# Kernel optimization log

Hardware: AMD Instinct MI355X
Metric: run time of the kernel (lower is better)

The kernel has to match this reference:

```python
import math
import jax, jax.numpy as jnp
import numpy as np

E = 256
HEADS = 8
WS = 8
BN_EPS = 1e-5


def pos_encoding_2d(embed_dim, H, W):
    d_half = embed_dim // 2
    div = jnp.exp(jnp.arange(0, d_half, 2, dtype=jnp.float32) * (-math.log(10000.0) / d_half))
    ang_h = jnp.arange(H, dtype=jnp.float32)[:, None] * div[None, :]  # [H, d_half//2]
    pe_h = jnp.zeros((H, d_half), jnp.float32).at[:, 0::2].set(jnp.sin(ang_h)).at[:, 1::2].set(jnp.cos(ang_h))
    ang_w = jnp.arange(W, dtype=jnp.float32)[:, None] * div[None, :]
    pe_w = jnp.zeros((W, d_half), jnp.float32).at[:, 0::2].set(jnp.sin(ang_w)).at[:, 1::2].set(jnp.cos(ang_w))
    pe = jnp.concatenate([
        jnp.broadcast_to(pe_h[:, None, :], (H, W, d_half)),
        jnp.broadcast_to(pe_w[None, :, :], (H, W, d_half)),
    ], axis=-1)  # [H, W, E]
    return jnp.transpose(pe, (2, 0, 1))[None]  # [1, E, H, W]


def window_partition(x, ws):
    # x: [B, E, H, W] -> [B*Hn*Wn, ws*ws, E]
    B, e, H, W = x.shape
    Hn, Wn = H // ws, W // ws
    x = x.reshape(B, e, Hn, ws, Wn, ws)
    x = jnp.transpose(x, (0, 2, 4, 3, 5, 1))  # [B, Hn, Wn, ws, ws, E]
    return x.reshape(B * Hn * Wn, ws * ws, e)


def window_reverse(x, B, H, W, ws):
    Hn, Wn = H // ws, W // ws
    e = x.shape[-1]
    x = x.reshape(B, Hn, Wn, ws, ws, e)
    x = jnp.transpose(x, (0, 5, 1, 3, 2, 4))  # [B, E, Hn, ws, Wn, ws]
    return x.reshape(B, e, H, W)


def setup_inputs() -> dict:
    key = jax.random.key(0)
    ks = jax.random.split(key, 16)
    B, H, W = 8, 128, 128
    in_ch = (512, 256, 256)
    s = lambda fan: 1.0 / np.sqrt(fan)
    return {
        "x5": jax.random.normal(ks[0], (B, in_ch[0], H, W), jnp.float32),
        "d1": jax.random.normal(ks[1], (B, in_ch[1], H, W), jnp.float32),
        "d2": jax.random.normal(ks[2], (B, in_ch[2], H, W), jnp.float32),
        "kp_w": jax.random.normal(ks[3], (E, in_ch[0]), jnp.float32) * s(in_ch[0]),
        "qp_w": jax.random.normal(ks[4], (E, in_ch[1]), jnp.float32) * s(in_ch[1]),
        "vp_w": jax.random.normal(ks[5], (E, in_ch[2]), jnp.float32) * s(in_ch[2]),
        "sp_w": jax.random.normal(ks[6], (E, in_ch[1]), jnp.float32) * s(in_ch[1]),
        "in_proj_w": jax.random.normal(ks[7], (3 * E, E), jnp.float32) * s(E),
        "in_proj_b": jnp.zeros((3 * E,), jnp.float32),
        "out_proj_w": jax.random.normal(ks[8], (E, E), jnp.float32) * s(E),
        "out_proj_b": jnp.zeros((E,), jnp.float32),
        "post_w": jax.random.normal(ks[9], (E, 2 * E, 3, 3), jnp.float32) * s(2 * E * 9),
        "gamma": jnp.ones((E,), jnp.float32),
        "beta": jnp.zeros((E,), jnp.float32),
    }


def reference(x5, d1, d2, kp_w, qp_w, vp_w, sp_w, in_proj_w, in_proj_b,
              out_proj_w, out_proj_b, post_w, gamma, beta):
    B, _, H, W = d1.shape
    pe = pos_encoding_2d(E, H, W)

    # 1x1 projections + positional encoding
    q = jnp.einsum('bchw,ec->behw', d1, qp_w) + pe
    k = jnp.einsum('bchw,ec->behw', x5, kp_w) + pe
    v = jnp.einsum('bchw,ec->behw', d2, vp_w) + pe

    # window partition -> [N, L, E]
    qw = window_partition(q, WS)
    kw = window_partition(k, WS)
    vw = window_partition(v, WS)
    N, L, _ = qw.shape
    hd = E // HEADS

    Wq, Wk, Wv = in_proj_w[:E], in_proj_w[E:2 * E], in_proj_w[2 * E:]
    bq, bk, bv = in_proj_b[:E], in_proj_b[E:2 * E], in_proj_b[2 * E:]
    qh = (qw @ Wq.T + bq).reshape(N, L, HEADS, hd)
    kh = (kw @ Wk.T + bk).reshape(N, L, HEADS, hd)
    vh = (vw @ Wv.T + bv).reshape(N, L, HEADS, hd)

    scale = 1.0 / math.sqrt(hd)
    scores = jnp.einsum('nqhd,nkhd->nhqk', qh, kh) * scale  # [N, heads, L, L]
    attn = jax.nn.softmax(scores, axis=-1)
    o = jnp.einsum('nhqk,nkhd->nqhd', attn, vh).reshape(N, L, E)
    o = o @ out_proj_w.T + out_proj_b

    attn_out = window_reverse(o, B, H, W, WS)  # [B, E, H, W]
    skip = jnp.einsum('bchw,ec->behw', d1, sp_w)

    y = jnp.concatenate([attn_out, skip], axis=1)  # [B, 2E, H, W]
    y = jax.lax.conv_general_dilated(
        y, post_w, window_strides=(1, 1), padding=((1, 1), (1, 1)),
        dimension_numbers=('NCHW', 'OIHW', 'NCHW'))
    # BatchNorm2d, training-mode batch statistics
    mean = jnp.mean(y, axis=(0, 2, 3), keepdims=True)
    var = jnp.var(y, axis=(0, 2, 3), keepdims=True)
    y = (y - mean) * jax.lax.rsqrt(var + BN_EPS)
    y = y * gamma[None, :, None, None] + beta[None, :, None, None]
    return jax.nn.relu(y)
```

## Files before the change

kernel.cpp:

```cpp
#include <hip/hip_runtime.h>
#include <cstdio>
#include <cmath>

typedef __attribute__((ext_vector_type(8))) short bf16x8;
typedef __attribute__((ext_vector_type(4))) float f32x4;

#define MFMA16(a, b, c) __builtin_amdgcn_mfma_f32_16x16x32_bf16((a), (b), (c), 0, 0, 0)

#define WSO_PE    0u
#define WSO_WQC   65536u
#define WSO_WKC   (WSO_WQC + 131072u)
#define WSO_WVC   (WSO_WKC + 262144u)
#define WSO_WSP   (WSO_WVC + 131072u)
#define WSO_WOP   (WSO_WSP + 131072u)
#define WSO_WC    (WSO_WOP + 131072u)
#define WSO_TB    (WSO_WC + 2359296u)
#define WSO_QH    (WSO_TB + 786432u)
#define WSO_KH    (WSO_QH + 67108864u)
#define WSO_VT    (WSO_KH + 67108864u)
#define WSO_YT    (WSO_VT + 67108864u)
#define WSO_SUMS  (WSO_YT + 134217728u)
#define WSO_SC    (WSO_SUMS + 2048u)
#define WSO_TOTAL (WSO_SC + 2048u)

#define SMEM_CONV 152064

__device__ __forceinline__ unsigned short f2b(float x) {
  unsigned int u = __builtin_bit_cast(unsigned int, x);
  u += 0x7fffu + ((u >> 16) & 1u);
  return (unsigned short)(u >> 16);
}

__device__ __forceinline__ bf16x8 rd8(const unsigned short* s, int row, int stride, int k) {
  return *reinterpret_cast<const bf16x8*>(s + row * stride + (k ^ ((row & 7) << 3)));
}

__global__ void k_prep(const float* __restrict__ spw, const float* __restrict__ opw,
                       const float* __restrict__ postw,
                       float* __restrict__ peT, unsigned short* __restrict__ wdst) {
  unsigned id = blockIdx.x * 256u + threadIdx.x;
  if (id < 16384u) {
    int p = id >> 7, j = id & 127;
    float div = expf(-9.210340371976184f * (float)(j & ~1) * (1.0f / 128.0f));
    float ang = (float)p * div;
    peT[id] = (j & 1) ? cosf(ang) : sinf(ang);
    return;
  }
  unsigned i = id - 16384u;
  if (i >= 1310720u) return;
  float v;
  if (i < 65536u)            v = spw[i];
  else if (i < 131072u)      v = opw[i - 65536u];
  else {
    unsigned r = i - 131072u;
    unsigned e = r & 7u, l = (r >> 3) & 63u, rt = (r >> 9) & 3u;
    unsigned idx3 = r >> 11;
    unsigned tap = idx3 % 9u, q = idx3 / 9u;
    unsigned ocb = q & 3u, cc = q >> 2;
    unsigned oc = ocb * 64u + rt * 16u + (l & 15u);
    unsigned ic = cc * 32u + (l >> 4) * 8u + e;
    v = postw[(oc * 512u + ic) * 9u + tap];
  }
  wdst[i] = f2b(v);
}

__global__ void k_fold(const float* __restrict__ qpw, const float* __restrict__ kpw,
                       const float* __restrict__ vpw, const float* __restrict__ inw,
                       const float* __restrict__ inb, const float* __restrict__ peT,
                       unsigned short* __restrict__ wqc, unsigned short* __restrict__ wkc,
                       unsigned short* __restrict__ wvc, float* __restrict__ tb) {
  __shared__ float wrow[256];
  const int tid = threadIdx.x, bid = blockIdx.x;
  if (bid < 768) {
    int m = bid >> 8;
    int e2 = bid & 255;
    wrow[tid] = inw[(m * 256 + e2) * 256 + tid];
    __syncthreads();
    if (m == 1) {
      float a0 = 0.f, a1 = 0.f;
      for (int e = 0; e < 256; ++e) {
        float s = wrow[e];
        a0 = fmaf(s, kpw[e * 512 + tid], a0);
        a1 = fmaf(s, kpw[e * 512 + 256 + tid], a1);
      }
      wkc[e2 * 512 + tid] = f2b(a0);
      wkc[e2 * 512 + 256 + tid] = f2b(a1);
    } else {
      const float* pw = (m == 0) ? qpw : vpw;
      float a0 = 0.f;
      for (int e = 0; e < 256; ++e) a0 = fmaf(wrow[e], pw[e * 256 + tid], a0);
      unsigned short* dst = (m == 0) ? wqc : wvc;
      dst[e2 * 256 + tid] = f2b(a0);
    }
  } else {
    int r = bid - 768;
    int t = r >> 7, p = r & 127;
    if (tid < 128) wrow[tid] = peT[p * 128 + tid];
    __syncthreads();
    int woff = (t >> 1) * 256, joff = (t & 1) * 128;
    float acc = (t & 1) ? 0.f : inb[woff + tid];
    const float* wr = inw + (size_t)(woff + tid) * 256 + joff;
    for (int j = 0; j < 128; ++j) acc = fmaf(wrow[j], wr[j], acc);
    tb[t * 32768 + p * 256 + tid] = acc;
  }
}

__device__ __forceinline__ void gemm4x4(f32x4 acc[4][4], const unsigned short* __restrict__ wA,
                                        int Kw, int kw0, const unsigned short* sB, int strideB,
                                        int nK, int wid, int lane) {
  const int rA = lane & 15;
  const int kq = (lane >> 4) << 3;
  for (int ks = 0; ks < nK; ks += 32) {
    bf16x8 a[4];
#pragma unroll
    for (int rt = 0; rt < 4; ++rt)
      a[rt] = *reinterpret_cast<const bf16x8*>(wA + (wid * 64 + rt * 16 + rA) * Kw + kw0 + ks + kq);
#pragma unroll
    for (int ct = 0; ct < 4; ++ct) {
      bf16x8 bb = rd8(sB, ct * 16 + rA, strideB, ks + kq);
#pragma unroll
      for (int rt = 0; rt < 4; ++rt) acc[rt][ct] = MFMA16(a[rt], bb, acc[rt][ct]);
    }
  }
}

__device__ __forceinline__ void stage128(unsigned short* sB, const float* __restrict__ src,
                                         int b, int Cin, int c0, int h0, int w0, int tid) {
  const int tok = tid & 63;
  const long base = ((long)(b * Cin + c0) << 14) + (h0 + (tok >> 3)) * 128 + w0 + (tok & 7);
  const int cb = (tid >> 6) << 3;
#pragma unroll
  for (int it = 0; it < 4; ++it) {
    const int c = cb + (it << 5);
    float v[8];
#pragma unroll
    for (int u = 0; u < 8; ++u) v[u] = src[base + ((long)(c + u) << 14)];
    bf16x8 pk;
#pragma unroll
    for (int u = 0; u < 8; ++u) ((unsigned short*)&pk)[u] = f2b(v[u]);
    *reinterpret_cast<bf16x8*>(&sB[(tok << 7) + (c ^ ((tok & 7) << 3))]) = pk;
  }
}

__device__ __forceinline__ void epi_qk(unsigned short* __restrict__ dst, const f32x4 acc[4][4],
                                       const float* __restrict__ At, const float* __restrict__ Bt,
                                       int h0, int w0, int wid, int lane) {
  const int gq = lane >> 4, l15 = lane & 15;
#pragma unroll
  for (int rt = 0; rt < 4; ++rt) {
    int e0 = wid * 64 + rt * 16 + gq * 4;
    int hd = e0 >> 5, chb = e0 & 31;
#pragma unroll
    for (int ct = 0; ct < 4; ++ct) {
      int tok = ct * 16 + l15;
      float4 av = *reinterpret_cast<const float4*>(At + (h0 + (tok >> 3)) * 256 + e0);
      float4 bv = *reinterpret_cast<const float4*>(Bt + (w0 + (tok & 7)) * 256 + e0);
      ushort4 pk;
      pk.x = f2b(acc[rt][ct][0] + av.x + bv.x);
      pk.y = f2b(acc[rt][ct][1] + av.y + bv.y);
      pk.z = f2b(acc[rt][ct][2] + av.z + bv.z);
      pk.w = f2b(acc[rt][ct][3] + av.w + bv.w);
      *reinterpret_cast<ushort4*>(dst + ((hd * 64 + tok) << 5) + chb) = pk;
    }
  }
}

__device__ __forceinline__ void epi_vT(unsigned short* __restrict__ dst, const f32x4 acc[4][4],
                                       const float* __restrict__ At, const float* __restrict__ Bt,
                                       int h0, int w0, int wid, int lane) {
  const int gq = lane >> 4, l15 = lane & 15;
#pragma unroll
  for (int rt = 0; rt < 4; ++rt) {
    int e0 = wid * 64 + rt * 16 + gq * 4;
    int hd = e0 >> 5, chb = e0 & 31;
#pragma unroll
    for (int ct = 0; ct < 4; ++ct) {
      int tok = ct * 16 + l15;
      float4 av = *reinterpret_cast<const float4*>(At + (h0 + (tok >> 3)) * 256 + e0);
      float4 bv = *reinterpret_cast<const float4*>(Bt + (w0 + (tok & 7)) * 256 + e0);
#pragma unroll
      for (int j = 0; j < 4; ++j) {
        float v = acc[rt][ct][j] + ((const float*)&av)[j] + ((const float*)&bv)[j];
        dst[((hd * 32 + chb + j) << 6) + tok] = f2b(v);
      }
    }
  }
}

__device__ __forceinline__ void epi_global(unsigned short* __restrict__ y_t, const f32x4 acc[4][4],
                                           const float* __restrict__ bias, int chOff,
                                           int b, int h0, int w0, int wid, int lane) {
#pragma unroll
  for (int rt = 0; rt < 4; ++rt) {
    int e0 = wid * 64 + rt * 16 + ((lane >> 4) << 2);
    float4 bs = bias ? *reinterpret_cast<const float4*>(bias + e0) : make_float4(0.f, 0.f, 0.f, 0.f);
    int ch = chOff + e0;
#pragma unroll
    for (int ct = 0; ct < 4; ++ct) {
      int tok = ct * 16 + (lane & 15);
      int r = tok >> 3, cpx = tok & 7;
      long gy = ((((long)(b * 16 + (ch >> 5)) * 128 + (h0 + r)) * 128 + (w0 + cpx)) << 5) + (ch & 31);
      ushort4 pk;
      pk.x = f2b(acc[rt][ct][0] + bs.x);
      pk.y = f2b(acc[rt][ct][1] + bs.y);
      pk.z = f2b(acc[rt][ct][2] + bs.z);
      pk.w = f2b(acc[rt][ct][3] + bs.w);
      *reinterpret_cast<ushort4*>(y_t + gy) = pk;
    }
  }
}

__launch_bounds__(256, 2)
__global__ void k_proj(const float* __restrict__ x5, const float* __restrict__ d1,
                       const float* __restrict__ d2,
                       const unsigned short* __restrict__ wqc, const unsigned short* __restrict__ wkc,
                       const unsigned short* __restrict__ wvc, const unsigned short* __restrict__ wsp,
                       const float* __restrict__ tb,
                       unsigned short* __restrict__ qh, unsigned short* __restrict__ kh,
                       unsigned short* __restrict__ vt, unsigned short* __restrict__ y_t) {
  __shared__ unsigned short sB[8192];
  const int tid = threadIdx.x, lane = tid & 63, wid = tid >> 6;
  const int bid = blockIdx.x;
  const int win = ((bid & 7) << 8) | (bid >> 3);
  const int b = win >> 8, wh = (win >> 4) & 15, ww = win & 15;
  const int h0 = wh * 8, w0 = ww * 8;

  const f32x4 vz = {0.f, 0.f, 0.f, 0.f};
  f32x4 accA[4][4], accB[4][4];

#pragma unroll
  for (int i = 0; i < 4; ++i)
#pragma unroll
    for (int j = 0; j < 4; ++j) { accA[i][j] = vz; accB[i][j] = vz; }
  for (int c0 = 0; c0 < 256; c0 += 128) {
    __syncthreads();
    stage128(sB, d1, b, 256, c0, h0, w0, tid);
    __syncthreads();
    gemm4x4(accA, wqc, 256, c0, sB, 128, 128, wid, lane);
    gemm4x4(accB, wsp, 256, c0, sB, 128, 128, wid, lane);
  }
  epi_qk(qh + ((size_t)win << 14), accA, tb, tb + 32768, h0, w0, wid, lane);
  epi_global(y_t, accB, nullptr, 256, b, h0, w0, wid, lane);

#pragma unroll
  for (int i = 0; i < 4; ++i)
#pragma unroll
    for (int j = 0; j < 4; ++j) accA[i][j] = vz;
  for (int c0 = 0; c0 < 512; c0 += 128) {
    __syncthreads();
    stage128(sB, x5, b, 512, c0, h0, w0, tid);
    __syncthreads();
    gemm4x4(accA, wkc, 512, c0, sB, 128, 128, wid, lane);
  }
  epi_qk(kh + ((size_t)win << 14), accA, tb + 65536, tb + 98304, h0, w0, wid, lane);

#pragma unroll
  for (int i = 0; i < 4; ++i)
#pragma unroll
    for (int j = 0; j < 4; ++j) accA[i][j] = vz;
  for (int c0 = 0; c0 < 256; c0 += 128) {
    __syncthreads();
    stage128(sB, d2, b, 256, c0, h0, w0, tid);
    __syncthreads();
    gemm4x4(accA, wvc, 256, c0, sB, 128, 128, wid, lane);
  }
  epi_vT(vt + ((size_t)win << 14), accA, tb + 131072, tb + 163840, h0, w0, wid, lane);
}

__launch_bounds__(256, 3)
__global__ void k_wattn(const unsigned short* __restrict__ qh, const unsigned short* __restrict__ kh,
                        const unsigned short* __restrict__ vt, const unsigned short* __restrict__ wop,
                        const float* __restrict__ out_b, unsigned short* __restrict__ y_t) {
  __shared__ unsigned short Pb[4096];
  __shared__ unsigned short bufO[16384];
  const int tid = threadIdx.x, lane = tid & 63, wid = tid >> 6;
  const int gq = lane >> 4, l15 = lane & 15, kq = gq << 3;
  const int bid = blockIdx.x;
  const int win = ((bid & 7) << 8) | (bid >> 3);
  const int b = win >> 8, wh = (win >> 4) & 15, ww = win & 15;
  const int h0 = wh * 8, w0 = ww * 8;

  const unsigned short* qw = qh + ((size_t)win << 14);
  const unsigned short* kw = kh + ((size_t)win << 14);
  const unsigned short* vw = vt + ((size_t)win << 14);

  const f32x4 vz = {0.f, 0.f, 0.f, 0.f};
  const float scl = 0.17677669529663687f;
  f32x4 o0[8], o1[8];
#pragma unroll
  for (int h = 0; h < 8; ++h) { o0[h] = vz; o1[h] = vz; }

#pragma unroll
  for (int hd = 0; hd < 8; ++hd) {
    const unsigned short* qb = qw + (hd << 11);
    const unsigned short* kb = kw + (hd << 11);
    const unsigned short* vb = vw + (hd << 11);
    bf16x8 aq = *reinterpret_cast<const bf16x8*>(qb + ((wid * 16 + l15) << 5) + kq);
    f32x4 sv[4];
#pragma unroll
    for (int ct = 0; ct < 4; ++ct) {
      bf16x8 bk = *reinterpret_cast<const bf16x8*>(kb + ((ct * 16 + l15) << 5) + kq);
      sv[ct] = MFMA16(aq, bk, vz);
    }
    float pr[4][4];
#pragma unroll
    for (int j = 0; j < 4; ++j) {
      float mx = fmaxf(fmaxf(sv[0][j], sv[1][j]), fmaxf(sv[2][j], sv[3][j])) * scl;
#pragma unroll
      for (int m = 8; m >= 1; m >>= 1) mx = fmaxf(mx, __shfl_xor(mx, m));
      float sum = 0.f;
#pragma unroll
      for (int ct = 0; ct < 4; ++ct) {
        float p = __expf(sv[ct][j] * scl - mx);
        pr[ct][j] = p;
        sum += p;
      }
#pragma unroll
      for (int m = 8; m >= 1; m >>= 1) sum += __shfl_xor(sum, m);
      float inv = 1.f / sum;
#pragma unroll
      for (int ct = 0; ct < 4; ++ct) pr[ct][j] *= inv;
    }
#pragma unroll
    for (int ct = 0; ct < 4; ++ct)
#pragma unroll
      for (int j = 0; j < 4; ++j) {
        int q = wid * 16 + gq * 4 + j;
        int kt = ct * 16 + l15;
        Pb[q * 64 + (kt ^ ((q & 7) << 3))] = f2b(pr[ct][j]);
      }
#pragma unroll
    for (int ks = 0; ks < 64; ks += 32) {
      bf16x8 bp = rd8(Pb, wid * 16 + l15, 64, ks + kq);
      bf16x8 a0 = *reinterpret_cast<const bf16x8*>(vb + (l15 << 6) + ks + kq);
      bf16x8 a1 = *reinterpret_cast<const bf16x8*>(vb + ((16 + l15) << 6) + ks + kq);
      o0[hd] = MFMA16(a0, bp, o0[hd]);
      o1[hd] = MFMA16(a1, bp, o1[hd]);
    }
  }

  {
    int tok = wid * 16 + l15;
    int sw = (tok & 7) << 3;
#pragma unroll
    for (int hd = 0; hd < 8; ++hd)
#pragma unroll
      for (int rt = 0; rt < 2; ++rt) {
        f32x4 ov = rt ? o1[hd] : o0[hd];
        int ch0 = hd * 32 + rt * 16 + gq * 4;
        ushort4 pk;
        pk.x = f2b(ov[0]); pk.y = f2b(ov[1]); pk.z = f2b(ov[2]); pk.w = f2b(ov[3]);
        *reinterpret_cast<ushort4*>(&bufO[tok * 256 + (ch0 ^ sw)]) = pk;
      }
  }
  __syncthreads();

  f32x4 accA[4][4];
#pragma unroll
  for (int i = 0; i < 4; ++i)
#pragma unroll
    for (int j = 0; j < 4; ++j) accA[i][j] = vz;
  gemm4x4(accA, wop, 256, 0, bufO, 256, 256, wid, lane);
  epi_global(y_t, accA, out_b, 0, b, h0, w0, wid, lane);
}

__device__ __forceinline__ void patch_load(const unsigned short* __restrict__ y_t,
                                           int b, int cc, int h0, int w0, int tid, uint4* pv) {
#pragma unroll
  for (int k = 0; k < 5; ++k) {
    int s = tid + (k << 9);
    uint4 v = make_uint4(0u, 0u, 0u, 0u);
    if (s < 2448) {
      int pr = (s * 482) >> 16;
      int rem = s - pr * 136;
      int pcpx = rem >> 2, g = rem & 3;
      int hh = h0 + pr - 1, wp = w0 + pcpx - 1;
      if ((unsigned)hh < 128u && (unsigned)wp < 128u)
        v = *reinterpret_cast<const uint4*>(
            y_t + ((((long)(b * 16 + cc) * 128 + hh) * 128 + wp) << 5) + (g << 3));
    }
    pv[k] = v;
  }
}

__device__ __forceinline__ void patch_store(unsigned short* buf, int tid, const uint4* pv) {
#pragma unroll
  for (int k = 0; k < 5; ++k) {
    int s = tid + (k << 9);
    if (s < 2448) {
      int pr = (s * 482) >> 16;
      int rem = s - pr * 136;
      int pcpx = rem >> 2, g = rem & 3;
      int pidx = pr * 34 + pcpx;
      *reinterpret_cast<uint4*>(buf + (pidx << 5) + ((g ^ ((pidx >> 1) & 3)) << 3)) = pv[k];
    }
  }
}

__device__ __forceinline__ void stage_A(const unsigned short* __restrict__ wA, int cc, int ocb,
                                        unsigned short* dstBase, int tid) {
  const unsigned short* src = wA + (size_t)(cc * 4 + ocb) * 18432 + tid * 8;
  unsigned short* dst = dstBase + tid * 8;
#pragma unroll
  for (int k = 0; k < 4; ++k) {
    __builtin_amdgcn_global_load_lds(
        (const __attribute__((address_space(1))) unsigned int*)(src + k * 4096),
        (__attribute__((address_space(3))) unsigned int*)(dst + k * 4096), 16, 0, 0);
  }
  if (tid < 256)
    __builtin_amdgcn_global_load_lds(
        (const __attribute__((address_space(1))) unsigned int*)(src + 16384),
        (__attribute__((address_space(3))) unsigned int*)(dst + 16384), 16, 0, 0);
}

__launch_bounds__(512, 2)
__global__ void k_conv(const unsigned short* __restrict__ y_t, const unsigned short* __restrict__ wc,
                       float* __restrict__ out) {
  extern __shared__ unsigned short cs[];
  unsigned short* Pb0 = cs;
  unsigned short* Pb1 = cs + 19584;
  unsigned short* Ab0 = cs + 39168;
  unsigned short* Ab1 = cs + 57600;

  const int tid = threadIdx.x, lane = tid & 63, pxg = tid >> 6;
  const int gq = lane >> 4, l15 = lane & 15;
  const int bi = ((int)blockIdx.x & 7) * 128 + ((int)blockIdx.x >> 3);
  const int ocb = bi & 3, wb = (bi >> 2) & 3, hb = (bi >> 4) & 7, b = bi >> 7;
  const int h0 = hb * 16, w0 = wb * 32;

  const f32x4 vz = {0.f, 0.f, 0.f, 0.f};
  f32x4 acc[4][4];
#pragma unroll
  for (int rt = 0; rt < 4; ++rt)
#pragma unroll
    for (int ct = 0; ct < 4; ++ct) acc[rt][ct] = vz;

  uint4 pv[5];
  patch_load(y_t, b, 0, h0, w0, tid, pv);
  stage_A(wc, 0, ocb, Ab0, tid);
  patch_store(Pb0, tid, pv);
  __syncthreads();

#pragma unroll 1
  for (int cc = 0; cc < 16; ++cc) {
    const unsigned short* pb = (cc & 1) ? Pb1 : Pb0;
    const unsigned short* pa = (cc & 1) ? Ab1 : Ab0;
    if (cc < 15) {
      patch_load(y_t, b, cc + 1, h0, w0, tid, pv);
      stage_A(wc, cc + 1, ocb, (cc & 1) ? Ab0 : Ab1, tid);
    }

#pragma unroll
    for (int kx = 0; kx < 3; ++kx) {
      bf16x8 bfr[4][2];
#pragma unroll
      for (int r = 0; r < 4; ++r)
#pragma unroll
        for (int ws = 0; ws < 2; ++ws) {
          int pidx = (pxg * 2 + r) * 34 + ws * 16 + l15 + kx;
          bfr[r][ws] = *reinterpret_cast<const bf16x8*>(
              pb + (pidx << 5) + ((gq ^ ((pidx >> 1) & 3)) << 3));
        }
      bf16x8 afr[3][4];
#pragma unroll
      for (int ky = 0; ky < 3; ++ky)
#pragma unroll
        for (int rt = 0; rt < 4; ++rt)
          afr[ky][rt] = *reinterpret_cast<const bf16x8*>(
              pa + (((ky * 3 + kx) * 4 + rt) << 9) + lane * 8);
#pragma unroll
      for (int ky = 0; ky < 3; ++ky)
#pragma unroll
        for (int ct = 0; ct < 4; ++ct) {
          int r = (ct >> 1) + ky, ws = ct & 1;
#pragma unroll
          for (int rt = 0; rt < 4; ++rt)
            acc[rt][ct] = MFMA16(afr[ky][rt], bfr[r][ws], acc[rt][ct]);
        }
    }

    if (cc < 15) patch_store((cc & 1) ? Pb0 : Pb1, tid, pv);
    __syncthreads();
  }

#pragma unroll
  for (int rt = 0; rt < 4; ++rt) {
    int oc0 = ocb * 64 + rt * 16 + gq * 4;
#pragma unroll
    for (int ct = 0; ct < 4; ++ct) {
      int hh = h0 + pxg * 2 + (ct >> 1), wp = w0 + ((ct & 1) << 4) + l15;
      long base = (((long)(b * 256 + oc0)) * 128 + hh) * 128 + wp;
#pragma unroll
      for (int j = 0; j < 4; ++j) out[base + (long)j * 16384] = acc[rt][ct][j];
    }
  }
}

__global__ void k_stats(const float* __restrict__ out, float* __restrict__ sums) {
  __shared__ float s1[256], s2[256];
  int c = blockIdx.x, tid = threadIdx.x;
  float a1 = 0.f, a2 = 0.f;
  for (int bb = 0; bb < 8; ++bb) {
    const float4* p = reinterpret_cast<const float4*>(out + ((long)(bb * 256 + c)) * 16384);
    for (int i = tid; i < 4096; i += 256) {
      float4 v = p[i];
      a1 += v.x + v.y + v.z + v.w;
      a2 += v.x * v.x + v.y * v.y + v.z * v.z + v.w * v.w;
    }
  }
  s1[tid] = a1; s2[tid] = a2;
  __syncthreads();
  for (int s = 128; s > 0; s >>= 1) {
    if (tid < s) { s1[tid] += s1[tid + s]; s2[tid] += s2[tid + s]; }
    __syncthreads();
  }
  if (tid == 0) { sums[c] = s1[0]; sums[256 + c] = s2[0]; }
}

__global__ void k_final(const float* __restrict__ sums, const float* __restrict__ gamma,
                        const float* __restrict__ beta, float* __restrict__ sc) {
  int c = threadIdx.x;
  float mean = sums[c] * (1.f / 131072.f);
  float var = sums[256 + c] * (1.f / 131072.f) - mean * mean;
  float s = gamma[c] * rsqrtf(var + 1e-5f);
  sc[c] = s;
  sc[256 + c] = beta[c] - mean * s;
}

__global__ void k_apply(float* __restrict__ out, const float* __restrict__ sc) {
  const long n4 = 33554432 / 4;
  for (long i4 = (long)blockIdx.x * 256 + threadIdx.x; i4 < n4; i4 += (long)gridDim.x * 256) {
    float4 v = reinterpret_cast<float4*>(out)[i4];
    int c = (int)((i4 >> 12) & 255);
    float s = sc[c], sh = sc[256 + c];
    v.x = fmaxf(v.x * s + sh, 0.f);
    v.y = fmaxf(v.y * s + sh, 0.f);
    v.z = fmaxf(v.z * s + sh, 0.f);
    v.w = fmaxf(v.w * s + sh, 0.f);
    reinterpret_cast<float4*>(out)[i4] = v;
  }
}

extern "C" void kernel_launch(void* const* d_in, const int* in_sizes, int n_in,
                              void* d_out, int out_size, void* d_ws, size_t ws_size,
                              hipStream_t stream) {
  const float* x5 = (const float*)d_in[0];
  const float* d1 = (const float*)d_in[1];
  const float* d2 = (const float*)d_in[2];
  const float* kp = (const float*)d_in[3];
  const float* qp = (const float*)d_in[4];
  const float* vp = (const float*)d_in[5];
  const float* spw = (const float*)d_in[6];
  const float* inw = (const float*)d_in[7];
  const float* inb = (const float*)d_in[8];
  const float* opw = (const float*)d_in[9];
  const float* opb = (const float*)d_in[10];
  const float* pw = (const float*)d_in[11];
  const float* gamma = (const float*)d_in[12];
  const float* beta = (const float*)d_in[13];

  if (ws_size < (size_t)WSO_TOTAL) {
    fprintf(stderr, "kernel_launch: ws too small: %zu < %u\n", ws_size, WSO_TOTAL);
    return;
  }

  char* ws = (char*)d_ws;
  float* peT = (float*)(ws + WSO_PE);
  unsigned short* w_qc = (unsigned short*)(ws + WSO_WQC);
  unsigned short* w_kc = (unsigned short*)(ws + WSO_WKC);
  unsigned short* w_vc = (unsigned short*)(ws + WSO_WVC);
  unsigned short* w_sp = (unsigned short*)(ws + WSO_WSP);
  unsigned short* w_op = (unsigned short*)(ws + WSO_WOP);
  unsigned short* w_c = (unsigned short*)(ws + WSO_WC);
  float* tb = (float*)(ws + WSO_TB);
  unsigned short* qh = (unsigned short*)(ws + WSO_QH);
  unsigned short* kh = (unsigned short*)(ws + WSO_KH);
  unsigned short* vt = (unsigned short*)(ws + WSO_VT);
  unsigned short* y_t = (unsigned short*)(ws + WSO_YT);
  float* sums = (float*)(ws + WSO_SUMS);
  float* sc = (float*)(ws + WSO_SC);

  hipFuncSetAttribute(reinterpret_cast<const void*>(k_conv),
                      hipFuncAttributeMaxDynamicSharedMemorySize, SMEM_CONV);

  k_prep<<<5184, 256, 0, stream>>>(spw, opw, pw, peT, w_sp);
  k_fold<<<1536, 256, 0, stream>>>(qp, kp, vp, inw, inb, peT, w_qc, w_kc, w_vc, tb);
  k_proj<<<2048, 256, 0, stream>>>(x5, d1, d2, w_qc, w_kc, w_vc, w_sp, tb, qh, kh, vt, y_t);
  k_wattn<<<2048, 256, 0, stream>>>(qh, kh, vt, w_op, opb, y_t);
  k_conv<<<1024, 512, SMEM_CONV, stream>>>(y_t, w_c, (float*)d_out);
  k_stats<<<256, 256, 0, stream>>>((const float*)d_out, sums);
  k_final<<<1, 256, 0, stream>>>(sums, gamma, beta, sc);
  k_apply<<<2048, 256, 0, stream>>>((float*)d_out, sc);
}
```

Before: 833.2 us.

## Restructure projection kernel into 1024-thread blocks with double-buffered staging and prepacked weights

Rewrites k_proj so each 1024-thread block handles a 8x32 token tile (four windows) for one projection sibling: Q, skip, K or V. Input activations are read with float4 loads and double-buffered in dynamic shared memory, so the next chunk's global load overlaps the MFMA work on the current one. Weights are pre-packed in k_prep and k_fold into the per-lane MFMA fragment order, giving contiguous A-fragment loads. This splits the work across more blocks and improves coalescing of the fp32 input reads. The cost is 64 KB of LDS per block, heavier register use at 1024 threads, and the K sibling doing twice the work of the others, which can leave the blocks unevenly loaded.

```diff
diff --git a/kernel.cpp b/kernel.cpp
--- a/kernel.cpp
+++ b/kernel.cpp
@@ -8,11 +8,10 @@
 #define MFMA16(a, b, c) __builtin_amdgcn_mfma_f32_16x16x32_bf16((a), (b), (c), 0, 0, 0)
 
 #define WSO_PE    0u
-#define WSO_WQC   65536u
-#define WSO_WKC   (WSO_WQC + 131072u)
-#define WSO_WVC   (WSO_WKC + 262144u)
-#define WSO_WSP   (WSO_WVC + 131072u)
-#define WSO_WOP   (WSO_WSP + 131072u)
+#define WSO_PWQS  65536u
+#define WSO_PWK   (WSO_PWQS + 262144u)
+#define WSO_PWV   (WSO_PWK + 262144u)
+#define WSO_WOP   (WSO_PWV + 131072u)
 #define WSO_WC    (WSO_WOP + 131072u)
 #define WSO_TB    (WSO_WC + 2359296u)
 #define WSO_QH    (WSO_TB + 786432u)
@@ -24,6 +23,7 @@
 #define WSO_TOTAL (WSO_SC + 2048u)
 
 #define SMEM_CONV 152064
+#define SMEM_PROJ 65536
 
 __device__ __forceinline__ unsigned short f2b(float x) {
   unsigned int u = __builtin_bit_cast(unsigned int, x);
@@ -35,9 +35,16 @@
   return *reinterpret_cast<const bf16x8*>(s + row * stride + (k ^ ((row & 7) << 3)));
 }
 
+__device__ __forceinline__ unsigned pack_idx(unsigned oc, unsigned ch, unsigned Mdiv) {
+  unsigned kc = ch >> 6, moG = oc >> 6, rt = (oc >> 4) & 3, ks = (ch >> 5) & 1;
+  unsigned l = (oc & 15) | (((ch >> 3) & 3) << 4), e = ch & 7;
+  return ((((kc * Mdiv + moG) * 4 + rt) * 2 + ks) * 64 + l) * 8 + e;
+}
+
 __global__ void k_prep(const float* __restrict__ spw, const float* __restrict__ opw,
                        const float* __restrict__ postw,
-                       float* __restrict__ peT, unsigned short* __restrict__ wdst) {
+                       float* __restrict__ peT, unsigned short* __restrict__ pwqs,
+                       unsigned short* __restrict__ wop, unsigned short* __restrict__ wc) {
   unsigned id = blockIdx.x * 256u + threadIdx.x;
   if (id < 16384u) {
     int p = id >> 7, j = id & 127;
@@ -48,10 +55,12 @@
   }
   unsigned i = id - 16384u;
   if (i >= 1310720u) return;
-  float v;
-  if (i < 65536u)            v = spw[i];
-  else if (i < 131072u)      v = opw[i - 65536u];
-  else {
+  if (i < 65536u) {
+    unsigned oc = i >> 8, ch = i & 255u;
+    pwqs[pack_idx(oc + 256u, ch, 8u)] = f2b(spw[i]);
+  } else if (i < 131072u) {
+    wop[i - 65536u] = f2b(opw[i - 65536u]);
+  } else {
     unsigned r = i - 131072u;
     unsigned e = r & 7u, l = (r >> 3) & 63u, rt = (r >> 9) & 3u;
     unsigned idx3 = r >> 11;
@@ -59,16 +68,15 @@
     unsigned ocb = q & 3u, cc = q >> 2;
     unsigned oc = ocb * 64u + rt * 16u + (l & 15u);
     unsigned ic = cc * 32u + (l >> 4) * 8u + e;
-    v = postw[(oc * 512u + ic) * 9u + tap];
-  }
-  wdst[i] = f2b(v);
+    wc[r] = f2b(postw[(oc * 512u + ic) * 9u + tap]);
+  }
 }
 
 __global__ void k_fold(const float* __restrict__ qpw, const float* __restrict__ kpw,
                        const float* __restrict__ vpw, const float* __restrict__ inw,
                        const float* __restrict__ inb, const float* __restrict__ peT,
-                       unsigned short* __restrict__ wqc, unsigned short* __restrict__ wkc,
-                       unsigned short* __restrict__ wvc, float* __restrict__ tb) {
+                       unsigned short* __restrict__ pwqs, unsigned short* __restrict__ pwk,
+                       unsigned short* __restrict__ pwv, float* __restrict__ tb) {
   __shared__ float wrow[256];
   const int tid = threadIdx.x, bid = blockIdx.x;
   if (bid < 768) {
@@ -83,14 +91,14 @@
         a0 = fmaf(s, kpw[e * 512 + tid], a0);
         a1 = fmaf(s, kpw[e * 512 + 256 + tid], a1);
       }
-      wkc[e2 * 512 + tid] = f2b(a0);
-      wkc[e2 * 512 + 256 + tid] = f2b(a1);
+      pwk[pack_idx(e2, tid, 4u)] = f2b(a0);
+      pwk[pack_idx(e2, tid + 256, 4u)] = f2b(a1);
     } else {
       const float* pw = (m == 0) ? qpw : vpw;
       float a0 = 0.f;
       for (int e = 0; e < 256; ++e) a0 = fmaf(wrow[e], pw[e * 256 + tid], a0);
-      unsigned short* dst = (m == 0) ? wqc : wvc;
-      dst[e2 * 256 + tid] = f2b(a0);
+      if (m == 0) pwqs[pack_idx(e2, tid, 8u)] = f2b(a0);
+      else        pwv[pack_idx(e2, tid, 4u)] = f2b(a0);
     }
   } else {
     int r = bid - 768;
@@ -124,69 +132,6 @@
   }
 }
 
-__device__ __forceinline__ void stage128(unsigned short* sB, const float* __restrict__ src,
-                                         int b, int Cin, int c0, int h0, int w0, int tid) {
-  const int tok = tid & 63;
-  const long base = ((long)(b * Cin + c0) << 14) + (h0 + (tok >> 3)) * 128 + w0 + (tok & 7);
-  const int cb = (tid >> 6) << 3;
-#pragma unroll
-  for (int it = 0; it < 4; ++it) {
-    const int c = cb + (it << 5);
-    float v[8];
-#pragma unroll
-    for (int u = 0; u < 8; ++u) v[u] = src[base + ((long)(c + u) << 14)];
-    bf16x8 pk;
-#pragma unroll
-    for (int u = 0; u < 8; ++u) ((unsigned short*)&pk)[u] = f2b(v[u]);
-    *reinterpret_cast<bf16x8*>(&sB[(tok << 7) + (c ^ ((tok & 7) << 3))]) = pk;
-  }
-}
-
-__device__ __forceinline__ void epi_qk(unsigned short* __restrict__ dst, const f32x4 acc[4][4],
-                                       const float* __restrict__ At, const float* __restrict__ Bt,
-                                       int h0, int w0, int wid, int lane) {
-  const int gq = lane >> 4, l15 = lane & 15;
-#pragma unroll
-  for (int rt = 0; rt < 4; ++rt) {
-    int e0 = wid * 64 + rt * 16 + gq * 4;
-    int hd = e0 >> 5, chb = e0 & 31;
-#pragma unroll
-    for (int ct = 0; ct < 4; ++ct) {
-      int tok = ct * 16 + l15;
-      float4 av = *reinterpret_cast<const float4*>(At + (h0 + (tok >> 3)) * 256 + e0);
-      float4 bv = *reinterpret_cast<const float4*>(Bt + (w0 + (tok & 7)) * 256 + e0);
-      ushort4 pk;
-      pk.x = f2b(acc[rt][ct][0] + av.x + bv.x);
-      pk.y = f2b(acc[rt][ct][1] + av.y + bv.y);
-      pk.z = f2b(acc[rt][ct][2] + av.z + bv.z);
-      pk.w = f2b(acc[rt][ct][3] + av.w + bv.w);
-      *reinterpret_cast<ushort4*>(dst + ((hd * 64 + tok) << 5) + chb) = pk;
-    }
-  }
-}
-
-__device__ __forceinline__ void epi_vT(unsigned short* __restrict__ dst, const f32x4 acc[4][4],
-                                       const float* __restrict__ At, const float* __restrict__ Bt,
-                                       int h0, int w0, int wid, int lane) {
-  const int gq = lane >> 4, l15 = lane & 15;
-#pragma unroll
-  for (int rt = 0; rt < 4; ++rt) {
-    int e0 = wid * 64 + rt * 16 + gq * 4;
-    int hd = e0 >> 5, chb = e0 & 31;
-#pragma unroll
-    for (int ct = 0; ct < 4; ++ct) {
-      int tok = ct * 16 + l15;
-      float4 av = *reinterpret_cast<const float4*>(At + (h0 + (tok >> 3)) * 256 + e0);
-      float4 bv = *reinterpret_cast<const float4*>(Bt + (w0 + (tok & 7)) * 256 + e0);
-#pragma unroll
-      for (int j = 0; j < 4; ++j) {
-        float v = acc[rt][ct][j] + ((const float*)&av)[j] + ((const float*)&bv)[j];
-        dst[((hd * 32 + chb + j) << 6) + tok] = f2b(v);
-      }
-    }
-  }
-}
-
 __device__ __forceinline__ void epi_global(unsigned short* __restrict__ y_t, const f32x4 acc[4][4],
                                            const float* __restrict__ bias, int chOff,
                                            int b, int h0, int w0, int wid, int lane) {
@@ -210,61 +155,161 @@
   }
 }
 
-__launch_bounds__(256, 2)
+__launch_bounds__(1024)
 __global__ void k_proj(const float* __restrict__ x5, const float* __restrict__ d1,
                        const float* __restrict__ d2,
-                       const unsigned short* __restrict__ wqc, const unsigned short* __restrict__ wkc,
-                       const unsigned short* __restrict__ wvc, const unsigned short* __restrict__ wsp,
-                       const float* __restrict__ tb,
+                       const unsigned short* __restrict__ pwqs, const unsigned short* __restrict__ pwk,
+                       const unsigned short* __restrict__ pwv, const float* __restrict__ tb,
                        unsigned short* __restrict__ qh, unsigned short* __restrict__ kh,
                        unsigned short* __restrict__ vt, unsigned short* __restrict__ y_t) {
-  __shared__ unsigned short sB[8192];
-  const int tid = threadIdx.x, lane = tid & 63, wid = tid >> 6;
-  const int bid = blockIdx.x;
-  const int win = ((bid & 7) << 8) | (bid >> 3);
-  const int b = win >> 8, wh = (win >> 4) & 15, ww = win & 15;
-  const int h0 = wh * 8, w0 = ww * 8;
+  extern __shared__ unsigned short sB[];
+  const int tid = threadIdx.x, l = tid & 63, wv = tid >> 6;
+  const int l15 = l & 15, gq = l >> 4;
+  const int braw = blockIdx.x;
+  const int bid = (braw & 7) * 256 + (braw >> 3);
+  const int sib = bid & 3, tile = bid >> 2;
+  const int wq = tile & 3, hs = (tile >> 2) & 15, b = tile >> 6;
+  const int h0 = hs * 8, w0 = wq * 32;
+  const int win = wv & 3, mo = wv >> 2;
+
+  const float* src; const unsigned short* wf; int Cin, nkc, Mdiv, moG;
+  if (sib == 0)      { src = d1; wf = pwqs; Cin = 256; nkc = 4; Mdiv = 8; moG = mo; }
+  else if (sib == 1) { src = d1; wf = pwqs; Cin = 256; nkc = 4; Mdiv = 8; moG = 4 + mo; }
+  else if (sib == 2) { src = x5; wf = pwk;  Cin = 512; nkc = 8; Mdiv = 4; moG = mo; }
+  else               { src = d2; wf = pwv;  Cin = 256; nkc = 4; Mdiv = 4; moG = mo; }
+
+  const int sq = l & 7, rbit = (l >> 3) & 1, cq = l >> 4;
+  const long srcb = ((long)(b * Cin) << 14) + (long)h0 * 128 + w0 + sq * 4;
+
+  int bOff[4];
+#pragma unroll
+  for (int ct = 0; ct < 4; ++ct) {
+    int wtok = ct * 16 + l15;
+    int tok = (wtok >> 3) * 32 + win * 8 + (wtok & 7);
+    int s = (tok ^ (tok >> 2)) & 7;
+    bOff[ct] = (tok << 6) + ((gq ^ s) << 3);
+  }
 
   const f32x4 vz = {0.f, 0.f, 0.f, 0.f};
-  f32x4 accA[4][4], accB[4][4];
-
-#pragma unroll
-  for (int i = 0; i < 4; ++i)
-#pragma unroll
-    for (int j = 0; j < 4; ++j) { accA[i][j] = vz; accB[i][j] = vz; }
-  for (int c0 = 0; c0 < 256; c0 += 128) {
+  f32x4 acc[4][4];
+#pragma unroll
+  for (int rt = 0; rt < 4; ++rt)
+#pragma unroll
+    for (int ct = 0; ct < 4; ++ct) acc[rt][ct] = vz;
+
+  float4 pv[4];
+  auto stage = [&](int kc) {
+#pragma unroll
+    for (int i = 0; i < 4; ++i) {
+      int c = ((wv & 7) << 3) + (cq << 1) + (i & 1);
+      int r = ((wv >> 3) << 2) + ((i >> 1) << 1) + rbit;
+      pv[i] = *reinterpret_cast<const float4*>(src + srcb + ((long)(kc * 64 + c) << 14) + r * 128);
+    }
+  };
+  auto wrt = [&](unsigned short* buf) {
+#pragma unroll
+    for (int i = 0; i < 4; ++i) {
+      int c = ((wv & 7) << 3) + (cq << 1) + (i & 1);
+      int r = ((wv >> 3) << 2) + ((i >> 1) << 1) + rbit;
+      int tok0 = (r << 5) + (sq << 2);
+      const float* f = reinterpret_cast<const float*>(&pv[i]);
+#pragma unroll
+      for (int e = 0; e < 4; ++e) {
+        int tok = tok0 + e;
+        int s = (tok ^ (tok >> 2)) & 7;
+        buf[(tok << 6) + ((((c >> 3) ^ s) << 3) | (c & 7))] = f2b(f[e]);
+      }
+    }
+  };
+
+  stage(0);
+  wrt(sB);
+  __syncthreads();
+
+#pragma unroll 1
+  for (int kc = 0; kc < nkc; ++kc) {
+    unsigned short* buf = sB + ((kc & 1) << 14);
+    if (kc + 1 < nkc) stage(kc + 1);
+    const unsigned short* pa = wf + (((kc * Mdiv + moG) << 12) | (l << 3));
+#pragma unroll
+    for (int ksi = 0; ksi < 2; ++ksi) {
+      bf16x8 a[4];
+#pragma unroll
+      for (int rt = 0; rt < 4; ++rt)
+        a[rt] = *reinterpret_cast<const bf16x8*>(pa + ((rt * 2 + ksi) << 9));
+#pragma unroll
+      for (int ct = 0; ct < 4; ++ct) {
+        bf16x8 bb = *reinterpret_cast<const bf16x8*>(buf + (bOff[ct] ^ (ksi << 5)));
+#pragma unroll
+        for (int rt = 0; rt < 4; ++rt) acc[rt][ct] = MFMA16(a[rt], bb, acc[rt][ct]);
+      }
+    }
+    if (kc + 1 < nkc) wrt(sB + (((kc + 1) & 1) << 14));
     __syncthreads();
-    stage128(sB, d1, b, 256, c0, h0, w0, tid);
-    __syncthreads();
-    gemm4x4(accA, wqc, 256, c0, sB, 128, 128, wid, lane);
-    gemm4x4(accB, wsp, 256, c0, sB, 128, 128, wid, lane);
-  }
-  epi_qk(qh + ((size_t)win << 14), accA, tb, tb + 32768, h0, w0, wid, lane);
-  epi_global(y_t, accB, nullptr, 256, b, h0, w0, wid, lane);
-
-#pragma unroll
-  for (int i = 0; i < 4; ++i)
-#pragma unroll
-    for (int j = 0; j < 4; ++j) accA[i][j] = vz;
-  for (int c0 = 0; c0 < 512; c0 += 128) {
-    __syncthreads();
-    stage128(sB, x5, b, 512, c0, h0, w0, tid);
-    __syncthreads();
-    gemm4x4(accA, wkc, 512, c0, sB, 128, 128, wid, lane);
-  }
-  epi_qk(kh + ((size_t)win << 14), accA, tb + 65536, tb + 98304, h0, w0, wid, lane);
-
-#pragma unroll
-  for (int i = 0; i < 4; ++i)
-#pragma unroll
-    for (int j = 0; j < 4; ++j) accA[i][j] = vz;
-  for (int c0 = 0; c0 < 256; c0 += 128) {
-    __syncthreads();
-    stage128(sB, d2, b, 256, c0, h0, w0, tid);
-    __syncthreads();
-    gemm4x4(accA, wvc, 256, c0, sB, 128, 128, wid, lane);
-  }
-  epi_vT(vt + ((size_t)win << 14), accA, tb + 131072, tb + 163840, h0, w0, wid, lane);
+  }
+
+  const int win_g = ((b * 16 + hs) << 4) + (wq << 2) + win;
+  if (sib == 0 || sib == 2) {
+    const float* At = tb + (sib == 0 ? 0 : 65536);
+    const float* Bt = tb + (sib == 0 ? 32768 : 98304);
+    unsigned short* dst = (sib == 0 ? qh : kh) + ((size_t)win_g << 14);
+#pragma unroll
+    for (int rt = 0; rt < 4; ++rt) {
+      int oc = mo * 64 + rt * 16 + gq * 4;
+#pragma unroll
+      for (int ct = 0; ct < 4; ++ct) {
+        int wtok = ct * 16 + l15;
+        int h = h0 + (wtok >> 3), wgl = w0 + win * 8 + (wtok & 7);
+        float4 av = *reinterpret_cast<const float4*>(At + h * 256 + oc);
+        float4 bv = *reinterpret_cast<const float4*>(Bt + wgl * 256 + oc);
+        ushort4 pk;
+        pk.x = f2b(acc[rt][ct][0] + av.x + bv.x);
+        pk.y = f2b(acc[rt][ct][1] + av.y + bv.y);
+        pk.z = f2b(acc[rt][ct][2] + av.z + bv.z);
+        pk.w = f2b(acc[rt][ct][3] + av.w + bv.w);
+        *reinterpret_cast<ushort4*>(dst + ((oc >> 5) << 11) + (wtok << 5) + (oc & 31)) = pk;
+      }
+    }
+  } else if (sib == 1) {
+#pragma unroll
+    for (int rt = 0; rt < 4; ++rt) {
+      int ch = 256 + mo * 64 + rt * 16 + gq * 4;
+      int cc = ch >> 5;
+#pragma unroll
+      for (int ct = 0; ct < 4; ++ct) {
+        int wtok = ct * 16 + l15;
+        int h = h0 + (wtok >> 3), wgl = w0 + win * 8 + (wtok & 7);
+        long gy = ((((long)(b * 16 + cc) * 128 + h) * 128 + wgl) << 5) + (ch & 31);
+        ushort4 pk;
+        pk.x = f2b(acc[rt][ct][0]);
+        pk.y = f2b(acc[rt][ct][1]);
+        pk.z = f2b(acc[rt][ct][2]);
+        pk.w = f2b(acc[rt][ct][3]);
+        *reinterpret_cast<ushort4*>(y_t + gy) = pk;
+      }
+    }
+  } else {
+    const float* At = tb + 131072;
+    const float* Bt = tb + 163840;
+    unsigned short* dst = vt + ((size_t)win_g << 14);
+#pragma unroll
+    for (int rt = 0; rt < 4; ++rt) {
+      int oc = mo * 64 + rt * 16 + gq * 4;
+      int hd = oc >> 5, chb = oc & 31;
+#pragma unroll
+      for (int ct = 0; ct < 4; ++ct) {
+        int wtok = ct * 16 + l15;
+        int h = h0 + (wtok >> 3), wgl = w0 + win * 8 + (wtok & 7);
+        float4 av = *reinterpret_cast<const float4*>(At + h * 256 + oc);
+        float4 bv = *reinterpret_cast<const float4*>(Bt + wgl * 256 + oc);
+        const float* avf = reinterpret_cast<const float*>(&av);
+        const float* bvf = reinterpret_cast<const float*>(&bv);
+#pragma unroll
+        for (int j = 0; j < 4; ++j)
+          dst[(hd << 11) + (chb + j) * 64 + wtok] = f2b(acc[rt][ct][j] + avf[j] + bvf[j]);
+      }
+    }
+  }
 }
 
 __launch_bounds__(256, 3)
@@ -566,10 +611,9 @@
 
   char* ws = (char*)d_ws;
   float* peT = (float*)(ws + WSO_PE);
-  unsigned short* w_qc = (unsigned short*)(ws + WSO_WQC);
-  unsigned short* w_kc = (unsigned short*)(ws + WSO_WKC);
-  unsigned short* w_vc = (unsigned short*)(ws + WSO_WVC);
-  unsigned short* w_sp = (unsigned short*)(ws + WSO_WSP);
+  unsigned short* pwqs = (unsigned short*)(ws + WSO_PWQS);
+  unsigned short* pwk = (unsigned short*)(ws + WSO_PWK);
+  unsigned short* pwv = (unsigned short*)(ws + WSO_PWV);
   unsigned short* w_op = (unsigned short*)(ws + WSO_WOP);
   unsigned short* w_c = (unsigned short*)(ws + WSO_WC);
   float* tb = (float*)(ws + WSO_TB);
@@ -582,10 +626,12 @@
 
   hipFuncSetAttribute(reinterpret_cast<const void*>(k_conv),
                       hipFuncAttributeMaxDynamicSharedMemorySize, SMEM_CONV);
-
-  k_prep<<<5184, 256, 0, stream>>>(spw, opw, pw, peT, w_sp);
-  k_fold<<<1536, 256, 0, stream>>>(qp, kp, vp, inw, inb, peT, w_qc, w_kc, w_vc, tb);
-  k_proj<<<2048, 256, 0, stream>>>(x5, d1, d2, w_qc, w_kc, w_vc, w_sp, tb, qh, kh, vt, y_t);
+  hipFuncSetAttribute(reinterpret_cast<const void*>(k_proj),
+                      hipFuncAttributeMaxDynamicSharedMemorySize, SMEM_PROJ);
+
+  k_prep<<<5184, 256, 0, stream>>>(spw, opw, pw, peT, pwqs, w_op, w_c);
+  k_fold<<<1536, 256, 0, stream>>>(qp, kp, vp, inw, inb, peT, pwqs, pwk, pwv, tb);
+  k_proj<<<2048, 1024, SMEM_PROJ, stream>>>(x5, d1, d2, pwqs, pwk, pwv, tb, qh, kh, vt, y_t);
   k_wattn<<<2048, 256, 0, stream>>>(qh, kh, vt, w_op, opb, y_t);
   k_conv<<<1024, 512, SMEM_CONV, stream>>>(y_t, w_c, (float*)d_out);
   k_stats<<<256, 256, 0, stream>>>((const float*)d_out, sums);
```

Result: slower. 960.2 us (+15.2%).
